# Kernel optimization log

Hardware: AMD Instinct MI355X
Metric: run time of the kernel (lower is better)

## Reference

```python
import jax, jax.numpy as jnp
import numpy as np

# Dims: lifted grid is N_X x N_Y, input signal has N_IN dims (= N_X*N_Y).
N_X, N_Y, N_IN = 32, 32, 1024
FILT = 33              # resolution-filter taps (odd, centered)
SIGMA0 = 0.1           # resolution_filter_initial_sigma (step 0 of decay schedule)
EPS = 1e-7


def _resolution_filter(sigma):
    # Gaussian taps on normalized coords in ~[-1, 1], normalized to sum 1.
    t = (jnp.arange(FILT, dtype=jnp.float32) - FILT // 2) * (2.0 / FILT)
    k = jnp.exp(-0.5 * jnp.square(t / sigma))
    return k / jnp.sum(k)


def _interpolate_lifting_map(lm_raw, filt):
    # Circular 1-D convolution of the generator parametrization with the
    # Gaussian resolution filter along the input-signal axis.
    P = N_X * N_Y
    pad = FILT // 2
    v = lm_raw.reshape(P, 1, N_IN)
    v = jnp.concatenate([v[..., -pad:], v, v[..., :pad]], axis=-1)  # wrap pad
    k = filt.reshape(1, 1, FILT)
    out = jax.lax.conv_general_dilated(
        v, k, window_strides=(1,), padding='VALID',
        dimension_numbers=('NCH', 'OIH', 'NCH'))
    return out.reshape(N_X, N_Y, N_IN)


def setup_inputs() -> dict:
    key = jax.random.key(0)
    k1, k2 = jax.random.split(key)
    x = jax.random.normal(k1, (16384, N_IN), dtype=jnp.float32)
    lm_raw = jax.random.normal(k2, (N_X, N_Y, N_IN), dtype=jnp.float32) / np.float32(np.sqrt(N_IN))
    return {"x": x, "lm_raw": lm_raw}


def reference(x, lm_raw):
    # _demean_and_normalize_input: per-sample demean + std-normalize.
    mu = jnp.mean(x, axis=-1, keepdims=True)
    sd = jnp.std(x, axis=-1, keepdims=True)
    xn = (x - mu) / (sd + EPS)
    # _sample_resolution_filter + _interpolate_lifting_map
    filt = _resolution_filter(jnp.asarray(SIGMA0, dtype=jnp.float32))
    lm = _interpolate_lifting_map(lm_raw, filt)  # [n_x, n_y, n_in]
    # _lift: y[b, i, j] = sum_n lm[i, j, n] * x[b, n]
    y = jnp.einsum('xyn,bn->bxy', lm, xn)
    return y
```

## Files before the change

### kernel.cpp

```cpp
#include <hip/hip_runtime.h>
#include <hip/hip_bf16.h>

#define N_IN   1024
#define N_P    1024
#define FILT   33
#define PAD    16

typedef __attribute__((ext_vector_type(8))) __bf16 bf16x8;
typedef __attribute__((ext_vector_type(4))) float  f32x4;

#define GLB(p) ((const __attribute__((address_space(1))) unsigned int*)(p))
#define LDSP(p) ((__attribute__((address_space(3))) unsigned int*)(p))

__device__ __forceinline__ unsigned short f2bf(float f) {
    union { __hip_bfloat16 h; unsigned short u; } cv;
    cv.h = __float2bfloat16(f);
    return cv.u;
}

__global__ __launch_bounds__(256)
void prep_kernel(const float* __restrict__ x, __hip_bfloat16* __restrict__ xn,
                 const float* __restrict__ lm_raw, __hip_bfloat16* __restrict__ lm,
                 int norm_blocks)
{
    __shared__ float rowbuf[N_IN];
    __shared__ float fw[FILT];
    const int tid = threadIdx.x;

    if (blockIdx.x < norm_blocks) {
        const int lane = tid & 63;
        const int row  = blockIdx.x * 4 + (tid >> 6);

        const float4* xr = reinterpret_cast<const float4*>(x + (size_t)row * N_IN);
        float4 v[4];
        float s = 0.f, s2 = 0.f;
#pragma unroll
        for (int i = 0; i < 4; i++) {
            v[i] = xr[i * 64 + lane];
            s  += v[i].x + v[i].y + v[i].z + v[i].w;
            s2 += v[i].x * v[i].x + v[i].y * v[i].y + v[i].z * v[i].z + v[i].w * v[i].w;
        }
#pragma unroll
        for (int off = 32; off > 0; off >>= 1) {
            s  += __shfl_xor(s,  off, 64);
            s2 += __shfl_xor(s2, off, 64);
        }
        const float mu  = s * (1.0f / N_IN);
        const float var = fmaxf(s2 * (1.0f / N_IN) - mu * mu, 0.0f);
        const float inv = 1.0f / (sqrtf(var) + 1e-7f);

        ushort4* outv = reinterpret_cast<ushort4*>(xn + (size_t)row * N_IN);
#pragma unroll
        for (int i = 0; i < 4; i++) {
            ushort4 o;
            o.x = f2bf((v[i].x - mu) * inv);
            o.y = f2bf((v[i].y - mu) * inv);
            o.z = f2bf((v[i].z - mu) * inv);
            o.w = f2bf((v[i].w - mu) * inv);
            outv[i * 64 + lane] = o;
        }
    } else {
        const int p = blockIdx.x - norm_blocks;

        if (tid < FILT) {
            float t = (tid - PAD) * (2.0f / FILT);
            float u = t * 10.0f;
            fw[tid] = expf(-0.5f * u * u);
        }
        reinterpret_cast<float4*>(rowbuf)[tid] =
            reinterpret_cast<const float4*>(lm_raw + (size_t)p * N_IN)[tid];
        __syncthreads();

        float fsum = 0.f;
#pragma unroll
        for (int f = 0; f < FILT; f++) fsum += fw[f];
        const float inv = 1.0f / fsum;

        const int n0 = tid * 4;
        float o[4] = {0.f, 0.f, 0.f, 0.f};
#pragma unroll
        for (int f = 0; f < FILT; f++) {
            const float w = fw[f];
#pragma unroll
            for (int j = 0; j < 4; j++)
                o[j] += w * rowbuf[(n0 + j + f - PAD) & (N_IN - 1)];
        }
        ushort4 ov;
        ov.x = f2bf(o[0] * inv);
        ov.y = f2bf(o[1] * inv);
        ov.z = f2bf(o[2] * inv);
        ov.w = f2bf(o[3] * inv);
        reinterpret_cast<ushort4*>(lm + (size_t)p * N_IN)[tid] = ov;
    }
}

__global__ __launch_bounds__(512, 2)
void gemm_big(const __hip_bfloat16* __restrict__ A,
              const __hip_bfloat16* __restrict__ B,
              float* __restrict__ C,
              int M, int N, int K)
{
    constexpr int BK = 32;
    __shared__ char smem[3][32768];

    const int tid = threadIdx.x;
    const int l   = tid & 63;
    const int w   = tid >> 6;
    const int wm  = w >> 2;
    const int wn  = w & 3;

    const int o    = blockIdx.x;
    const int lin  = (o & 7) * (gridDim.x >> 3) + (o >> 3);
    const int tn   = lin & 3;
    const int tm   = lin >> 2;
    const size_t bm = (size_t)tm * 256;
    const size_t bn = (size_t)tn * 256;

    const int srow = w * 16 + (l >> 2);
    const int scol = 16 * ((l & 3) ^ ((l >> 3) & 3));
    const char* gA = (const char*)(A + (bm + srow) * (size_t)K) + scol;
    const char* gB = (const char*)(B + (bn + srow) * (size_t)K) + scol;
    const size_t rowstep = (size_t)128 * K * 2;

#define STAGE(t, b) do {                                                        \
    const char* a0_ = gA + (size_t)(t) * (BK * 2);                              \
    const char* b0_ = gB + (size_t)(t) * (BK * 2);                              \
    char* La_ = &smem[(b)][0]     + w * 1024;                                   \
    char* Lb_ = &smem[(b)][16384] + w * 1024;                                   \
    __builtin_amdgcn_global_load_lds(GLB(a0_),           LDSP(La_),        16, 0, 0); \
    __builtin_amdgcn_global_load_lds(GLB(a0_ + rowstep), LDSP(La_ + 8192), 16, 0, 0); \
    __builtin_amdgcn_global_load_lds(GLB(b0_),           LDSP(Lb_),        16, 0, 0); \
    __builtin_amdgcn_global_load_lds(GLB(b0_ + rowstep), LDSP(Lb_ + 8192), 16, 0, 0); \
} while (0)

    const int lr = l & 15;
    const int kb = l >> 4;
    const int rslot = 16 * (kb ^ ((lr >> 1) & 3));
    const int abase = (wm * 128 + lr) * 64 + rslot;
    const int bbase = 16384 + (wn * 64 + lr) * 64 + rslot;

    f32x4 acc[8][4] = {};
    const int NT = K / BK;

    STAGE(0, 0);
    STAGE(1, 1);

    int buf = 0;
    for (int t = 0; t < NT; ++t) {
        asm volatile("s_waitcnt lgkmcnt(0)" ::: "memory");
        if (t < NT - 1) asm volatile("s_waitcnt vmcnt(4)" ::: "memory");
        else            asm volatile("s_waitcnt vmcnt(0)" ::: "memory");
        __builtin_amdgcn_s_barrier();
        __builtin_amdgcn_sched_barrier(0);

        {
            const int t2 = t + 2;
            if (t2 < NT) {
                int b2 = buf + 2; if (b2 >= 3) b2 -= 3;
                STAGE(t2, b2);
            }
        }

        const char* Sb = &smem[buf][0];
        bf16x8 bfr[4], afr[4], afr2[4];
#pragma unroll
        for (int n = 0; n < 4; n++) bfr[n]  = *(const bf16x8*)(Sb + bbase + n * 1024);
#pragma unroll
        for (int m = 0; m < 4; m++) afr[m]  = *(const bf16x8*)(Sb + abase + m * 1024);

        __builtin_amdgcn_s_setprio(1);
#pragma unroll
        for (int m = 0; m < 4; m++)
#pragma unroll
            for (int n = 0; n < 4; n++)
                acc[m][n] = __builtin_amdgcn_mfma_f32_16x16x32_bf16(afr[m], bfr[n], acc[m][n], 0, 0, 0);
        __builtin_amdgcn_s_setprio(0);

#pragma unroll
        for (int m = 0; m < 4; m++) afr2[m] = *(const bf16x8*)(Sb + abase + (m + 4) * 1024);

        __builtin_amdgcn_s_setprio(1);
#pragma unroll
        for (int m = 0; m < 4; m++)
#pragma unroll
            for (int n = 0; n < 4; n++)
                acc[m + 4][n] = __builtin_amdgcn_mfma_f32_16x16x32_bf16(afr2[m], bfr[n], acc[m + 4][n], 0, 0, 0);
        __builtin_amdgcn_s_setprio(0);

        if (++buf == 3) buf = 0;
    }
#undef STAGE

    const int crow = (l >> 4) * 4;
    const int ccol = l & 15;
#pragma unroll
    for (int m = 0; m < 8; m++)
#pragma unroll
        for (int n = 0; n < 4; n++) {
#pragma unroll
            for (int r = 0; r < 4; r++) {
                const size_t row = bm + wm * 128 + m * 16 + crow + r;
                const size_t col = bn + wn * 64 + n * 16 + ccol;
                C[row * N + col] = acc[m][n][r];
            }
        }
}

extern "C" void kernel_launch(void* const* d_in, const int* in_sizes, int n_in,
                              void* d_out, int out_size, void* d_ws, size_t ws_size,
                              hipStream_t stream) {
    const float* x      = (const float*)d_in[0];
    const float* lm_raw = (const float*)d_in[1];
    float* out = (float*)d_out;

    const int M = in_sizes[0] / N_IN;

    __hip_bfloat16* xn = (__hip_bfloat16*)d_ws;
    __hip_bfloat16* lm = (__hip_bfloat16*)((char*)d_ws + (size_t)M * N_IN * 2);

    const int norm_blocks = M / 4;
    prep_kernel<<<norm_blocks + N_P, 256, 0, stream>>>(x, xn, lm_raw, lm, norm_blocks);

    const int nblk = (M / 256) * (N_P / 256);
    gemm_big<<<nblk, dim3(512), 0, stream>>>(xn, lm, out, M, N_P, N_IN);
}
```

Measured before the change: 63.60 us.

## Unroll GEMM main loop by two with 4-deep LDS ring, one barrier per pair

The bf16 MFMA GEMM now uses four LDS stage buffers instead of three and processes two K-steps per loop iteration. This needs only one workgroup barrier per pair of steps, cutting barrier and synchronisation overhead while keeping more global-to-LDS loads in flight. The vmcnt waits now come after the barrier. Each wave therefore only waits on its own loads before reading tiles that other waves filled, which risks reading LDS data that is not ready yet. LDS use grows to 128KB per block.

```diff
diff --git a/kernel.cpp b/kernel.cpp
--- a/kernel.cpp
+++ b/kernel.cpp
@@ -95,13 +95,13 @@
 }
 
 __global__ __launch_bounds__(512, 2)
-void gemm_big(const __hip_bfloat16* __restrict__ A,
-              const __hip_bfloat16* __restrict__ B,
-              float* __restrict__ C,
-              int M, int N, int K)
+void gemm_pair(const __hip_bfloat16* __restrict__ A,
+               const __hip_bfloat16* __restrict__ B,
+               float* __restrict__ C,
+               int M, int N, int K)
 {
     constexpr int BK = 32;
-    __shared__ char smem[3][32768];
+    __shared__ char smem[4][32768];
 
     const int tid = threadIdx.x;
     const int l   = tid & 63;
@@ -133,6 +133,31 @@
     __builtin_amdgcn_global_load_lds(GLB(b0_ + rowstep), LDSP(Lb_ + 8192), 16, 0, 0); \
 } while (0)
 
+#define COMPUTE(b) do {                                                         \
+    const char* Sb_ = &smem[(b)][0];                                            \
+    bf16x8 bfr[4], afr[4], afr2[4];                                             \
+    _Pragma("unroll")                                                           \
+    for (int n = 0; n < 4; n++) bfr[n]  = *(const bf16x8*)(Sb_ + bbase + n * 1024); \
+    _Pragma("unroll")                                                           \
+    for (int m = 0; m < 4; m++) afr[m]  = *(const bf16x8*)(Sb_ + abase + m * 1024); \
+    __builtin_amdgcn_s_setprio(1);                                              \
+    _Pragma("unroll")                                                           \
+    for (int m = 0; m < 4; m++)                                                 \
+        _Pragma("unroll")                                                       \
+        for (int n = 0; n < 4; n++)                                             \
+            acc[m][n] = __builtin_amdgcn_mfma_f32_16x16x32_bf16(afr[m], bfr[n], acc[m][n], 0, 0, 0); \
+    __builtin_amdgcn_s_setprio(0);                                              \
+    _Pragma("unroll")                                                           \
+    for (int m = 0; m < 4; m++) afr2[m] = *(const bf16x8*)(Sb_ + abase + (m + 4) * 1024); \
+    __builtin_amdgcn_s_setprio(1);                                              \
+    _Pragma("unroll")                                                           \
+    for (int m = 0; m < 4; m++)                                                 \
+        _Pragma("unroll")                                                       \
+        for (int n = 0; n < 4; n++)                                             \
+            acc[m + 4][n] = __builtin_amdgcn_mfma_f32_16x16x32_bf16(afr2[m], bfr[n], acc[m + 4][n], 0, 0, 0); \
+    __builtin_amdgcn_s_setprio(0);                                              \
+} while (0)
+
     const int lr = l & 15;
     const int kb = l >> 4;
     const int rslot = 16 * (kb ^ ((lr >> 1) & 3));
@@ -145,51 +170,25 @@
     STAGE(0, 0);
     STAGE(1, 1);
 
-    int buf = 0;
-    for (int t = 0; t < NT; ++t) {
+    for (int t = 0; t < NT; t += 2) {
         asm volatile("s_waitcnt lgkmcnt(0)" ::: "memory");
-        if (t < NT - 1) asm volatile("s_waitcnt vmcnt(4)" ::: "memory");
-        else            asm volatile("s_waitcnt vmcnt(0)" ::: "memory");
         __builtin_amdgcn_s_barrier();
+        asm volatile("" ::: "memory");
         __builtin_amdgcn_sched_barrier(0);
 
-        {
-            const int t2 = t + 2;
-            if (t2 < NT) {
-                int b2 = buf + 2; if (b2 >= 3) b2 -= 3;
-                STAGE(t2, b2);
-            }
-        }
-
-        const char* Sb = &smem[buf][0];
-        bf16x8 bfr[4], afr[4], afr2[4];
-#pragma unroll
-        for (int n = 0; n < 4; n++) bfr[n]  = *(const bf16x8*)(Sb + bbase + n * 1024);
-#pragma unroll
-        for (int m = 0; m < 4; m++) afr[m]  = *(const bf16x8*)(Sb + abase + m * 1024);
-
-        __builtin_amdgcn_s_setprio(1);
-#pragma unroll
-        for (int m = 0; m < 4; m++)
-#pragma unroll
-            for (int n = 0; n < 4; n++)
-                acc[m][n] = __builtin_amdgcn_mfma_f32_16x16x32_bf16(afr[m], bfr[n], acc[m][n], 0, 0, 0);
-        __builtin_amdgcn_s_setprio(0);
-
-#pragma unroll
-        for (int m = 0; m < 4; m++) afr2[m] = *(const bf16x8*)(Sb + abase + (m + 4) * 1024);
-
-        __builtin_amdgcn_s_setprio(1);
-#pragma unroll
-        for (int m = 0; m < 4; m++)
-#pragma unroll
-            for (int n = 0; n < 4; n++)
-                acc[m + 4][n] = __builtin_amdgcn_mfma_f32_16x16x32_bf16(afr2[m], bfr[n], acc[m + 4][n], 0, 0, 0);
-        __builtin_amdgcn_s_setprio(0);
-
-        if (++buf == 3) buf = 0;
+        if (t + 2 < NT) STAGE(t + 2, (t + 2) & 3);
+        if (t + 2 < NT) asm volatile("s_waitcnt vmcnt(8)" ::: "memory");
+        else            asm volatile("s_waitcnt vmcnt(4)" ::: "memory");
+        COMPUTE(t & 3);
+
+        if (t + 3 < NT) STAGE(t + 3, (t + 3) & 3);
+        if (t + 3 < NT)      asm volatile("s_waitcnt vmcnt(8)" ::: "memory");
+        else if (t + 2 < NT) asm volatile("s_waitcnt vmcnt(4)" ::: "memory");
+        else                 asm volatile("s_waitcnt vmcnt(0)" ::: "memory");
+        COMPUTE((t + 1) & 3);
     }
 #undef STAGE
+#undef COMPUTE
 
     const int crow = (l >> 4) * 4;
     const int ccol = l & 15;
@@ -222,5 +221,5 @@
     prep_kernel<<<norm_blocks + N_P, 256, 0, stream>>>(x, xn, lm_raw, lm, norm_blocks);
 
     const int nblk = (M / 256) * (N_P / 256);
-    gemm_big<<<nblk, dim3(512), 0, stream>>>(xn, lm, out, M, N_P, N_IN);
-}
+    gemm_pair<<<nblk, dim3(512), 0, stream>>>(xn, lm, out, M, N_P, N_IN);
+}
```

Result: faster. 62.35 us, median of 3 (-2.0%).
